# Kernel optimization log

Hardware: AMD Instinct MI355X
Metric: run time of the kernel (lower is better)

The kernel has to match this reference:

```python
import jax, jax.numpy as jnp
import numpy as np

G = 17          # joint groups == deform_groups == conv groups
BN_EPS = 1e-5   # torch BatchNorm2d default eps


def setup_inputs() -> dict:
    key = jax.random.key(0)
    ks = jax.random.split(key, 4)
    B, C, H, W = 4, 544, 96, 96
    Cg = C // G
    x = jax.random.normal(ks[0], (B, C, H, W), jnp.float32)
    # small std so sampled offsets stay a few pixels (realistic post-training scale)
    w_off = jax.random.normal(ks[1], (6 * G, Cg, 3, 3), jnp.float32) * 0.01
    b_off = jnp.zeros((6 * G,), jnp.float32)
    w_def = jax.random.normal(ks[2], (C, Cg, 3, 3), jnp.float32) * 0.05
    gamma = jnp.ones((C,), jnp.float32)
    beta = jnp.zeros((C,), jnp.float32)
    run_mean = jnp.zeros((C,), jnp.float32)
    run_var = jnp.ones((C,), jnp.float32)
    return dict(x=x, w_off=w_off, b_off=b_off, w_def=w_def, gamma=gamma,
                beta=beta, run_mean=run_mean, run_var=run_var)


def _forward(x, w_off, b_off, w_def, gamma, beta, run_mean, run_var):
    B, C, H, W = x.shape
    Cg = C // G
    residual = x
    # --- offset generation: grouped 3x3 conv -> per-pixel 2x3 affine per group ---
    t = jax.lax.conv_general_dilated(
        x, w_off, window_strides=(1, 1), padding=((1, 1), (1, 1)),
        dimension_numbers=('NCHW', 'OIHW', 'NCHW'), feature_group_count=G)
    t = t + b_off[None, :, None, None]
    aff = t.transpose(0, 2, 3, 1).reshape(B, H, W, G, 2, 3)   # [B,H,W,G,2,3]
    # regular 3x3 grid in homogeneous coords: rows = (dy, dx, 1), 9 taps row-major
    reg = jnp.array([[-1, -1, -1, 0, 0, 0, 1, 1, 1],
                     [-1, 0, 1, -1, 0, 1, -1, 0, 1],
                     [1, 1, 1, 1, 1, 1, 1, 1, 1]], jnp.float32)
    off = jnp.einsum('bhwgrt,tk->bhwgrk', aff, reg)           # [B,H,W,G,2,9]
    off = off.transpose(0, 3, 5, 1, 2, 4)                     # [B,G,9,H,W,2]
    offy = off[..., 0]                                        # [B,G,9,H,W]
    offx = off[..., 1]
    # --- deformable conv: bilinear-sampled gather at offset grid taps ---
    ky = jnp.array([-1, -1, -1, 0, 0, 0, 1, 1, 1], jnp.float32)
    kx = jnp.array([-1, 0, 1, -1, 0, 1, -1, 0, 1], jnp.float32)
    hh = jnp.arange(H, dtype=jnp.float32)
    ww = jnp.arange(W, dtype=jnp.float32)
    py = hh[None, None, None, :, None] + ky[None, None, :, None, None] + offy
    px = ww[None, None, None, None, :] + kx[None, None, :, None, None] + offx
    xf = x.reshape(B, G, Cg, H * W)
    y0 = jnp.floor(py)
    x0 = jnp.floor(px)
    sampled = jnp.zeros((B, G, Cg, 9, H, W), x.dtype)
    for dy in (0.0, 1.0):
        for dx in (0.0, 1.0):
            yc = y0 + dy
            xc = x0 + dx
            wgt = (1.0 - jnp.abs(py - yc)) * (1.0 - jnp.abs(px - xc))
            valid = ((yc >= 0) & (yc < H) & (xc >= 0) & (xc < W)).astype(x.dtype)
            yi = jnp.clip(yc, 0, H - 1).astype(jnp.int32)
            xi = jnp.clip(xc, 0, W - 1).astype(jnp.int32)
            idx = (yi * W + xi).reshape(B, G, 1, 9 * H * W)
            v = jnp.take_along_axis(xf, idx, axis=3).reshape(B, G, Cg, 9, H, W)
            sampled = sampled + v * (wgt * valid)[:, :, None]
    wg = w_def.reshape(G, C // G, Cg, 9)                      # [G, Cout/G, Cin/G, 9]
    out = jnp.einsum('bgikhw,goik->bgohw', sampled, wg).reshape(B, C, H, W)
    # --- eval-mode BatchNorm2d + residual ReLU ---
    inv = jax.lax.rsqrt(run_var + BN_EPS)
    out = (out - run_mean[None, :, None, None]) * (inv * gamma)[None, :, None, None] \
          + beta[None, :, None, None]
    return jax.nn.relu(out + residual)


def reference(x, w_off, b_off, w_def, gamma, beta, run_mean, run_var):
    return _forward(x, w_off, b_off, w_def, gamma, beta, run_mean, run_var)
```

## Files before the change

kernel.cpp:

```cpp
#include <hip/hip_runtime.h>
#include <math.h>

#define G  17
#define Cg 32
#define B  4
#define C  544
#define H  96
#define W  96
#define HW (H*W)
#define TILES 36
#define NBLK (B*G*TILES)
#define BN_EPS 1e-5f

typedef float    f32x4  __attribute__((ext_vector_type(4)));
typedef short    short8 __attribute__((ext_vector_type(8)));
typedef _Float16 h2     __attribute__((ext_vector_type(2)));
typedef _Float16 h8     __attribute__((ext_vector_type(8)));

#define WIN       22
#define HALO      3
#define WPOS      (WIN*WIN)
#define W_STRIDE  80
#define W_BYTES   (WPOS*W_STRIDE)
#define B_STRIDE  592
#define B_BYTES   (Cg*B_STRIDE)
#define WO_BYTES  (6*B_STRIDE)
#define SMEM_BYTES (W_BYTES + B_BYTES + WO_BYTES)

__device__ __forceinline__ int swizzle_blk(int blk) {
    return (blk & 7) * (NBLK / 8) + (blk >> 3);
}

__global__ __launch_bounds__(256) void transpose_kernel(
    const float* __restrict__ x, _Float16* __restrict__ xT)
{
    __shared__ float t[256*33];
    const int blk  = swizzle_blk(blockIdx.x);
    const int tile = blk % TILES;
    const int g    = (blk / TILES) % G;
    const int b    = blk / (TILES*G);

    const float* xg = x + ((size_t)b*C + g*Cg)*HW + tile*256;
    #pragma unroll
    for (int i = 0; i < Cg; ++i)
        t[threadIdx.x*33 + i] = xg[(size_t)i*HW + threadIdx.x];
    __syncthreads();

    h8* dst = (h8*)(xT + ((size_t)(b*G + g)*HW + (size_t)tile*256)*Cg);
    #pragma unroll
    for (int r = 0; r < 4; ++r) {
        const int idx = r*256 + threadIdx.x;
        const float* s = &t[(idx >> 2)*33 + (idx & 3)*8];
        h8 o;
        #pragma unroll
        for (int j = 0; j < 8; ++j) o[j] = (_Float16)s[j];
        dst[idx] = o;
    }
}

__global__ __launch_bounds__(256) void fused_deform_kernel(
    const float* __restrict__ x, const _Float16* __restrict__ xT,
    const float* __restrict__ w_off, const float* __restrict__ b_off,
    const float* __restrict__ w_def, const float* __restrict__ gamma,
    const float* __restrict__ beta, const float* __restrict__ rmean,
    const float* __restrict__ rvar, float* __restrict__ out)
{
    __shared__ __align__(16) char smem[SMEM_BYTES];
    char* Wsm  = smem;
    char* Bsm  = smem + W_BYTES;
    char* Wo   = smem + W_BYTES + B_BYTES;
    char* AffS = Wo;

    const int blk  = swizzle_blk(blockIdx.x);
    const int tile = blk % TILES;
    const int g    = (blk / TILES) % G;
    const int b    = blk / (TILES*G);
    const int ty   = tile / 6, tx = tile % 6;
    const int h0   = ty*16,    w0 = tx*16;
    const int tid  = threadIdx.x;
    const int lane = tid & 63;
    const int wv   = tid >> 6;
    const int r15  = lane & 15;
    const int koff = lane >> 4;
    const int kb   = koff*16;

    const _Float16* xgT_base = xT + (size_t)(b*G + g)*HW*Cg;

    for (int i = tid; i < WPOS*4; i += 256) {
        const int pos = i >> 2, ch = (i & 3)*8;
        const int wy = pos / WIN, wx = pos % WIN;
        const int y  = h0 + wy - HALO, xx = w0 + wx - HALO;
        short8 v = (short8){0,0,0,0,0,0,0,0};
        if (((unsigned)y < H) && ((unsigned)xx < W))
            v = *(const short8*)(xgT_base + ((size_t)y*W + xx)*Cg + ch);
        *(short8*)(Wsm + pos*W_STRIDE + ch*2) = v;
    }
    for (int l = tid; l < Cg*288; l += 256) {
        const int o = l / 288, K = l % 288;
        const int t = K >> 5, i = K & 31;
        const float wt = w_def[(size_t)(g*Cg + o)*(Cg*9) + i*9 + t];
        *(_Float16*)(Bsm + o*B_STRIDE + K*2) = (_Float16)wt;
    }
    for (int l = tid; l < 6*288; l += 256) {
        const int o = l / 288, K = l % 288;
        const int t = K >> 5, i = K & 31;
        const float wt = w_off[(size_t)(g*6 + o)*288 + i*9 + t];
        *(_Float16*)(Wo + o*B_STRIDE + K*2) = (_Float16)wt;
    }
    __syncthreads();

    f32x4 acc_off[4];
    #pragma unroll
    for (int m = 0; m < 4; ++m) acc_off[m] = (f32x4){0.f, 0.f, 0.f, 0.f};

    #pragma unroll
    for (int t = 0; t < 9; ++t) {
        const int dy = t/3 - 1, dx = t%3 - 1;
        h8 bo = (h8){0,0,0,0,0,0,0,0};
        if (r15 < 6) bo = *(const h8*)(Wo + r15*B_STRIDE + t*64 + kb);
        #pragma unroll
        for (int m = 0; m < 4; ++m) {
            const int wr = wv*4 + m + dy + HALO;
            const int wc = r15 + dx + HALO;
            const h8 a = *(const h8*)(Wsm + (wr*WIN + wc)*W_STRIDE + kb);
            acc_off[m] = __builtin_amdgcn_mfma_f32_16x16x32_f16(a, bo, acc_off[m], 0, 0, 0);
        }
    }
    __syncthreads();

    if (r15 < 6) {
        #pragma unroll
        for (int m = 0; m < 4; ++m)
            #pragma unroll
            for (int r = 0; r < 4; ++r) {
                const int lp = (wv*4 + m)*16 + koff*4 + r;
                *(_Float16*)(AffS + lp*12 + r15*2) = (_Float16)acc_off[m][r];
            }
    }
    __syncthreads();

    const float bo0 = b_off[g*6+0], bo1 = b_off[g*6+1], bo2 = b_off[g*6+2];
    const float bo3 = b_off[g*6+3], bo4 = b_off[g*6+4], bo5 = b_off[g*6+5];
    float a0p[4], a1v[4], a2w[4], a3v[4], a4p[4], a5w[4];
    #pragma unroll
    for (int m = 0; m < 4; ++m) {
        const int row = wv*4 + m;
        const int lp = row*16 + r15;
        const h2 p01 = *(const h2*)(AffS + lp*12);
        const h2 p23 = *(const h2*)(AffS + lp*12 + 4);
        const h2 p45 = *(const h2*)(AffS + lp*12 + 8);
        a0p[m] = (float)p01[0] + bo0 + 1.0f;
        a1v[m] = (float)p01[1] + bo1;
        a2w[m] = (float)p23[0] + bo2 + (float)(row + HALO);
        a3v[m] = (float)p23[1] + bo3;
        a4p[m] = (float)p45[0] + bo4 + 1.0f;
        a5w[m] = (float)p45[1] + bo5 + (float)(r15 + HALO);
    }

    f32x4 acc[4][2];
    #pragma unroll
    for (int m = 0; m < 4; ++m)
        #pragma unroll
        for (int n = 0; n < 2; ++n)
            acc[m][n] = (f32x4){0.f, 0.f, 0.f, 0.f};

    #pragma unroll 1
    for (int t = 0; t < 9; ++t) {
        const float kyf = (float)(t/3 - 1);
        const float kxf = (float)(t%3 - 1);

        h8 af[4];
        #pragma unroll
        for (int m = 0; m < 4; ++m) {
            const float pyw = fmaf(a0p[m], kyf, fmaf(a1v[m], kxf, a2w[m]));
            const float pxw = fmaf(a3v[m], kyf, fmaf(a4p[m], kxf, a5w[m]));
            const float y0f = floorf(pyw), x0f = floorf(pxw);
            const float fy = pyw - y0f,   fx = pxw - x0f;
            int iy = (int)y0f, ix = (int)x0f;
            iy = min(max(iy, 0), WIN-2);
            ix = min(max(ix, 0), WIN-2);
            const float gy = 1.0f - fy, gx = 1.0f - fx;
            const float w00 = gy*gx, w01 = gy*fx, w10 = fy*gx, w11 = fy*fx;
            const _Float16 h00 = (_Float16)w00, h01 = (_Float16)w01;
            const _Float16 h10 = (_Float16)w10, h11 = (_Float16)w11;
            const h2 W00 = (h2){h00, h00}, W01 = (h2){h01, h01};
            const h2 W10 = (h2){h10, h10}, W11 = (h2){h11, h11};

            const char* base = Wsm + (iy*WIN + ix)*W_STRIDE + kb;
            union { short8 s; h2 h[4]; h8 v; } u00, u01, u10, u11, r;
            u00.s = *(const short8*)(base);
            u01.s = *(const short8*)(base + W_STRIDE);
            u10.s = *(const short8*)(base + WIN*W_STRIDE);
            u11.s = *(const short8*)(base + WIN*W_STRIDE + W_STRIDE);

            #pragma unroll
            for (int j = 0; j < 4; ++j)
                r.h[j] = W00*u00.h[j] + W01*u01.h[j] + W10*u10.h[j] + W11*u11.h[j];
            af[m] = r.v;
        }

        #pragma unroll
        for (int n = 0; n < 2; ++n) {
            const h8 bf = *(const h8*)(Bsm + (n*16 + r15)*B_STRIDE + t*64 + kb);
            #pragma unroll
            for (int m = 0; m < 4; ++m)
                acc[m][n] = __builtin_amdgcn_mfma_f32_16x16x32_f16(af[m], bf, acc[m][n], 0, 0, 0);
        }
    }

    float scl[2], shf[2];
    #pragma unroll
    for (int n = 0; n < 2; ++n) {
        const int c = g*Cg + n*16 + r15;
        const float inv = rsqrtf(rvar[c] + BN_EPS);
        scl[n] = inv * gamma[c];
        shf[n] = beta[c] - rmean[c]*scl[n];
    }
    #pragma unroll
    for (int m = 0; m < 4; ++m) {
        const int row = wv*4 + m;
        const int pxg = (h0 + row)*W + w0 + koff*4;
        #pragma unroll
        for (int n = 0; n < 2; ++n) {
            const int c = g*Cg + n*16 + r15;
            const size_t base = ((size_t)b*C + c)*HW + pxg;
            const float4 res = *(const float4*)(x + base);
            float4 ov;
            ov.x = fmaxf(fmaf(acc[m][n][0], scl[n], shf[n]) + res.x, 0.0f);
            ov.y = fmaxf(fmaf(acc[m][n][1], scl[n], shf[n]) + res.y, 0.0f);
            ov.z = fmaxf(fmaf(acc[m][n][2], scl[n], shf[n]) + res.z, 0.0f);
            ov.w = fmaxf(fmaf(acc[m][n][3], scl[n], shf[n]) + res.w, 0.0f);
            *(float4*)(out + base) = ov;
        }
    }
}

__global__ __launch_bounds__(256) void offset_conv_kernel(
    const float* __restrict__ x, const float* __restrict__ w_off,
    const float* __restrict__ b_off, float* __restrict__ aff)
{
    __shared__ float wl[Cg*9*6];
    const int blk  = swizzle_blk(blockIdx.x);
    const int tile = blk % TILES;
    const int g    = (blk / TILES) % G;
    const int b    = blk / (TILES*G);

    for (int l = threadIdx.x; l < Cg*9*6; l += 256) {
        int c = l % 6; int t = (l/6) % 9; int i = l/54;
        wl[l] = w_off[(size_t)(g*6 + c)*(Cg*9) + i*9 + t];
    }
    __syncthreads();

    const int p = tile*256 + threadIdx.x;
    const int h = p / W, w = p % W;

    float acc[6];
    #pragma unroll
    for (int c = 0; c < 6; ++c) acc[c] = b_off[g*6 + c];

    const float* xg = x + ((size_t)b*C + g*Cg)*HW;
    for (int i = 0; i < Cg; ++i) {
        const float* xc = xg + (size_t)i*HW;
        #pragma unroll
        for (int t = 0; t < 9; ++t) {
            const int dy = t/3 - 1, dx = t%3 - 1;
            const int yy = h + dy, xx = w + dx;
            float v = (yy >= 0 && yy < H && xx >= 0 && xx < W) ? xc[yy*W + xx] : 0.0f;
            #pragma unroll
            for (int c = 0; c < 6; ++c)
                acc[c] = fmaf(v, wl[(i*9 + t)*6 + c], acc[c]);
        }
    }

    float* ap = aff + ((size_t)(b*G + g)*6)*HW + p;
    #pragma unroll
    for (int c = 0; c < 6; ++c) ap[(size_t)c*HW] = acc[c];
}

__global__ __launch_bounds__(256) void deform_conv_kernel(
    const float* __restrict__ x, const float* __restrict__ w_def,
    const float* __restrict__ aff, const float* __restrict__ gamma,
    const float* __restrict__ beta, const float* __restrict__ rmean,
    const float* __restrict__ rvar, float* __restrict__ out)
{
    __shared__ float wl[9*Cg*Cg];
    const int blk  = swizzle_blk(blockIdx.x);
    const int tile = blk % TILES;
    const int g    = (blk / TILES) % G;
    const int b    = blk / (TILES*G);

    for (int l = threadIdx.x; l < 9*Cg*Cg; l += 256) {
        int o = l & 31; int i = (l >> 5) & 31; int k = l >> 10;
        wl[l] = w_def[(size_t)(g*Cg + o)*(Cg*9) + i*9 + k];
    }
    __syncthreads();

    const int p = tile*256 + threadIdx.x;
    const int h = p / W, w = p % W;

    const float* ap = aff + ((size_t)(b*G + g)*6)*HW + p;
    const float a0 = ap[0*(size_t)HW], a1 = ap[1*(size_t)HW], a2 = ap[2*(size_t)HW];
    const float a3 = ap[3*(size_t)HW], a4 = ap[4*(size_t)HW], a5 = ap[5*(size_t)HW];

    float acc[Cg];
    #pragma unroll
    for (int o = 0; o < Cg; ++o) acc[o] = 0.0f;

    const float* xg = x + ((size_t)b*C + g*Cg)*HW;

    #pragma unroll
    for (int k = 0; k < 9; ++k) {
        const float kyf = (float)(k/3 - 1);
        const float kxf = (float)(k%3 - 1);
        const float offy = a0*kyf + a1*kxf + a2;
        const float offx = a3*kyf + a4*kxf + a5;
        const float py = (float)h + kyf + offy;
        const float px = (float)w + kxf + offx;
        const float y0f = floorf(py), x0f = floorf(px);
        const float fy = py - y0f,   fx = px - x0f;
        const int y0 = (int)y0f, x0 = (int)x0f;
        const int y1 = y0 + 1,   x1 = x0 + 1;
        const bool vy0 = (y0 >= 0) && (y0 < H);
        const bool vy1 = (y1 >= 0) && (y1 < H);
        const bool vx0 = (x0 >= 0) && (x0 < W);
        const bool vx1 = (x1 >= 0) && (x1 < W);
        const float w00 = (vy0 && vx0) ? (1.0f - fy)*(1.0f - fx) : 0.0f;
        const float w01 = (vy0 && vx1) ? (1.0f - fy)*fx          : 0.0f;
        const float w10 = (vy1 && vx0) ? fy*(1.0f - fx)          : 0.0f;
        const float w11 = (vy1 && vx1) ? fy*fx                   : 0.0f;
        const int y0c = min(max(y0, 0), H-1), y1c = min(max(y1, 0), H-1);
        const int x0c = min(max(x0, 0), W-1), x1c = min(max(x1, 0), W-1);
        const int p00 = y0c*W + x0c, p01 = y0c*W + x1c;
        const int p10 = y1c*W + x0c, p11 = y1c*W + x1c;

        const float* wk = &wl[k*Cg*Cg];
        for (int i = 0; i < Cg; ++i) {
            const float* xc = xg + (size_t)i*HW;
            const float v = w00*xc[p00] + w01*xc[p01] + w10*xc[p10] + w11*xc[p11];
            #pragma unroll
            for (int o = 0; o < Cg; ++o)
                acc[o] = fmaf(v, wk[i*Cg + o], acc[o]);
        }
    }

    float* op = out + ((size_t)b*C + g*Cg)*HW + p;
    #pragma unroll
    for (int o = 0; o < Cg; ++o) {
        const int c = g*Cg + o;
        const float inv = rsqrtf(rvar[c] + BN_EPS);
        float val = (acc[o] - rmean[c]) * (inv * gamma[c]) + beta[c];
        val += xg[(size_t)o*HW + p];
        op[(size_t)o*HW] = fmaxf(val, 0.0f);
    }
}

extern "C" void kernel_launch(void* const* d_in, const int* in_sizes, int n_in,
                              void* d_out, int out_size, void* d_ws, size_t ws_size,
                              hipStream_t stream) {
    const float* x     = (const float*)d_in[0];
    const float* w_off = (const float*)d_in[1];
    const float* b_off = (const float*)d_in[2];
    const float* w_def = (const float*)d_in[3];
    const float* gamma = (const float*)d_in[4];
    const float* beta  = (const float*)d_in[5];
    const float* rmean = (const float*)d_in[6];
    const float* rvar  = (const float*)d_in[7];
    float* out = (float*)d_out;

    const size_t XT_BYTES  = (size_t)B*G*HW*Cg*sizeof(_Float16);
    const size_t AFF_BYTES = (size_t)B*G*6*HW*sizeof(float);

    if (ws_size >= XT_BYTES) {
        _Float16* xT = (_Float16*)d_ws;
        transpose_kernel<<<NBLK, 256, 0, stream>>>(x, xT);
        fused_deform_kernel<<<NBLK, 256, 0, stream>>>(x, xT, w_off, b_off,
                                                      w_def, gamma, beta,
                                                      rmean, rvar, out);
    } else if (ws_size >= AFF_BYTES) {
        float* aff = (float*)d_ws;
        offset_conv_kernel<<<NBLK, 256, 0, stream>>>(x, w_off, b_off, aff);
        deform_conv_kernel<<<NBLK, 256, 0, stream>>>(x, w_def, aff, gamma, beta,
                                                     rmean, rvar, out);
    }
}
```

Before: 114.1 us.

## Fuse NCHW-to-fp16 window staging into deform kernel, drop transpose pass

Removes the separate transpose kernel that wrote an fp16 channel-last copy of x to workspace. The fused kernel now loads the halo window straight from NCHW fp32 x with float4 row reads, converts to fp16 and scatters into the channel-interleaved shared layout. The aim is to save one kernel launch and a full write plus reread of the transposed tensor. In exchange, shared-memory stores become scattered 2-byte writes that may bank-conflict, and halo pixels are reread from fp32 by neighbouring tiles. The fallback two-kernel path is deleted.

```diff
diff --git a/kernel.cpp b/kernel.cpp
--- a/kernel.cpp
+++ b/kernel.cpp
@@ -31,39 +31,12 @@
     return (blk & 7) * (NBLK / 8) + (blk >> 3);
 }
 
-__global__ __launch_bounds__(256) void transpose_kernel(
-    const float* __restrict__ x, _Float16* __restrict__ xT)
-{
-    __shared__ float t[256*33];
-    const int blk  = swizzle_blk(blockIdx.x);
-    const int tile = blk % TILES;
-    const int g    = (blk / TILES) % G;
-    const int b    = blk / (TILES*G);
-
-    const float* xg = x + ((size_t)b*C + g*Cg)*HW + tile*256;
-    #pragma unroll
-    for (int i = 0; i < Cg; ++i)
-        t[threadIdx.x*33 + i] = xg[(size_t)i*HW + threadIdx.x];
-    __syncthreads();
-
-    h8* dst = (h8*)(xT + ((size_t)(b*G + g)*HW + (size_t)tile*256)*Cg);
-    #pragma unroll
-    for (int r = 0; r < 4; ++r) {
-        const int idx = r*256 + threadIdx.x;
-        const float* s = &t[(idx >> 2)*33 + (idx & 3)*8];
-        h8 o;
-        #pragma unroll
-        for (int j = 0; j < 8; ++j) o[j] = (_Float16)s[j];
-        dst[idx] = o;
-    }
-}
-
 __global__ __launch_bounds__(256) void fused_deform_kernel(
-    const float* __restrict__ x, const _Float16* __restrict__ xT,
-    const float* __restrict__ w_off, const float* __restrict__ b_off,
-    const float* __restrict__ w_def, const float* __restrict__ gamma,
-    const float* __restrict__ beta, const float* __restrict__ rmean,
-    const float* __restrict__ rvar, float* __restrict__ out)
+    const float* __restrict__ x, const float* __restrict__ w_off,
+    const float* __restrict__ b_off, const float* __restrict__ w_def,
+    const float* __restrict__ gamma, const float* __restrict__ beta,
+    const float* __restrict__ rmean, const float* __restrict__ rvar,
+    float* __restrict__ out)
 {
     __shared__ __align__(16) char smem[SMEM_BYTES];
     char* Wsm  = smem;
@@ -84,16 +57,34 @@
     const int koff = lane >> 4;
     const int kb   = koff*16;
 
-    const _Float16* xgT_base = xT + (size_t)(b*G + g)*HW*Cg;
-
-    for (int i = tid; i < WPOS*4; i += 256) {
-        const int pos = i >> 2, ch = (i & 3)*8;
-        const int wy = pos / WIN, wx = pos % WIN;
-        const int y  = h0 + wy - HALO, xx = w0 + wx - HALO;
-        short8 v = (short8){0,0,0,0,0,0,0,0};
-        if (((unsigned)y < H) && ((unsigned)xx < W))
-            v = *(const short8*)(xgT_base + ((size_t)y*W + xx)*Cg + ch);
-        *(short8*)(Wsm + pos*W_STRIDE + ch*2) = v;
+    const float* xg = x + ((size_t)b*C + g*Cg)*HW;
+
+    for (int i = tid; i < 32*22*6; i += 256) {
+        const int ch  = i / 132;
+        const int rem = i - ch*132;
+        const int wy  = rem / 6;
+        const int seg = rem - wy*6;
+        const int y   = h0 + wy - HALO;
+        const int cb  = w0 - 4 + seg*4;
+        f32x4 v = (f32x4){0.f, 0.f, 0.f, 0.f};
+        if ((unsigned)y < H) {
+            if (cb >= 0 && cb + 3 < W) {
+                v = *(const f32x4*)(xg + (size_t)ch*HW + y*W + cb);
+            } else {
+                const float* row = xg + (size_t)ch*HW + y*W;
+                #pragma unroll
+                for (int j = 0; j < 4; ++j) {
+                    const int c = cb + j;
+                    if ((unsigned)c < W) v[j] = row[c];
+                }
+            }
+        }
+        #pragma unroll
+        for (int j = 0; j < 4; ++j) {
+            const int wx = seg*4 + j - 1;
+            if ((unsigned)wx < WIN)
+                *(_Float16*)(Wsm + (wy*WIN + wx)*W_STRIDE + ch*2) = (_Float16)v[j];
+        }
     }
     for (int l = tid; l < Cg*288; l += 256) {
         const int o = l / 288, K = l % 288;
@@ -235,125 +226,6 @@
     }
 }
 
-__global__ __launch_bounds__(256) void offset_conv_kernel(
-    const float* __restrict__ x, const float* __restrict__ w_off,
-    const float* __restrict__ b_off, float* __restrict__ aff)
-{
-    __shared__ float wl[Cg*9*6];
-    const int blk  = swizzle_blk(blockIdx.x);
-    const int tile = blk % TILES;
-    const int g    = (blk / TILES) % G;
-    const int b    = blk / (TILES*G);
-
-    for (int l = threadIdx.x; l < Cg*9*6; l += 256) {
-        int c = l % 6; int t = (l/6) % 9; int i = l/54;
-        wl[l] = w_off[(size_t)(g*6 + c)*(Cg*9) + i*9 + t];
-    }
-    __syncthreads();
-
-    const int p = tile*256 + threadIdx.x;
-    const int h = p / W, w = p % W;
-
-    float acc[6];
-    #pragma unroll
-    for (int c = 0; c < 6; ++c) acc[c] = b_off[g*6 + c];
-
-    const float* xg = x + ((size_t)b*C + g*Cg)*HW;
-    for (int i = 0; i < Cg; ++i) {
-        const float* xc = xg + (size_t)i*HW;
-        #pragma unroll
-        for (int t = 0; t < 9; ++t) {
-            const int dy = t/3 - 1, dx = t%3 - 1;
-            const int yy = h + dy, xx = w + dx;
-            float v = (yy >= 0 && yy < H && xx >= 0 && xx < W) ? xc[yy*W + xx] : 0.0f;
-            #pragma unroll
-            for (int c = 0; c < 6; ++c)
-                acc[c] = fmaf(v, wl[(i*9 + t)*6 + c], acc[c]);
-        }
-    }
-
-    float* ap = aff + ((size_t)(b*G + g)*6)*HW + p;
-    #pragma unroll
-    for (int c = 0; c < 6; ++c) ap[(size_t)c*HW] = acc[c];
-}
-
-__global__ __launch_bounds__(256) void deform_conv_kernel(
-    const float* __restrict__ x, const float* __restrict__ w_def,
-    const float* __restrict__ aff, const float* __restrict__ gamma,
-    const float* __restrict__ beta, const float* __restrict__ rmean,
-    const float* __restrict__ rvar, float* __restrict__ out)
-{
-    __shared__ float wl[9*Cg*Cg];
-    const int blk  = swizzle_blk(blockIdx.x);
-    const int tile = blk % TILES;
-    const int g    = (blk / TILES) % G;
-    const int b    = blk / (TILES*G);
-
-    for (int l = threadIdx.x; l < 9*Cg*Cg; l += 256) {
-        int o = l & 31; int i = (l >> 5) & 31; int k = l >> 10;
-        wl[l] = w_def[(size_t)(g*Cg + o)*(Cg*9) + i*9 + k];
-    }
-    __syncthreads();
-
-    const int p = tile*256 + threadIdx.x;
-    const int h = p / W, w = p % W;
-
-    const float* ap = aff + ((size_t)(b*G + g)*6)*HW + p;
-    const float a0 = ap[0*(size_t)HW], a1 = ap[1*(size_t)HW], a2 = ap[2*(size_t)HW];
-    const float a3 = ap[3*(size_t)HW], a4 = ap[4*(size_t)HW], a5 = ap[5*(size_t)HW];
-
-    float acc[Cg];
-    #pragma unroll
-    for (int o = 0; o < Cg; ++o) acc[o] = 0.0f;
-
-    const float* xg = x + ((size_t)b*C + g*Cg)*HW;
-
-    #pragma unroll
-    for (int k = 0; k < 9; ++k) {
-        const float kyf = (float)(k/3 - 1);
-        const float kxf = (float)(k%3 - 1);
-        const float offy = a0*kyf + a1*kxf + a2;
-        const float offx = a3*kyf + a4*kxf + a5;
-        const float py = (float)h + kyf + offy;
-        const float px = (float)w + kxf + offx;
-        const float y0f = floorf(py), x0f = floorf(px);
-        const float fy = py - y0f,   fx = px - x0f;
-        const int y0 = (int)y0f, x0 = (int)x0f;
-        const int y1 = y0 + 1,   x1 = x0 + 1;
-        const bool vy0 = (y0 >= 0) && (y0 < H);
-        const bool vy1 = (y1 >= 0) && (y1 < H);
-        const bool vx0 = (x0 >= 0) && (x0 < W);
-        const bool vx1 = (x1 >= 0) && (x1 < W);
-        const float w00 = (vy0 && vx0) ? (1.0f - fy)*(1.0f - fx) : 0.0f;
-        const float w01 = (vy0 && vx1) ? (1.0f - fy)*fx          : 0.0f;
-        const float w10 = (vy1 && vx0) ? fy*(1.0f - fx)          : 0.0f;
-        const float w11 = (vy1 && vx1) ? fy*fx                   : 0.0f;
-        const int y0c = min(max(y0, 0), H-1), y1c = min(max(y1, 0), H-1);
-        const int x0c = min(max(x0, 0), W-1), x1c = min(max(x1, 0), W-1);
-        const int p00 = y0c*W + x0c, p01 = y0c*W + x1c;
-        const int p10 = y1c*W + x0c, p11 = y1c*W + x1c;
-
-        const float* wk = &wl[k*Cg*Cg];
-        for (int i = 0; i < Cg; ++i) {
-            const float* xc = xg + (size_t)i*HW;
-            const float v = w00*xc[p00] + w01*xc[p01] + w10*xc[p10] + w11*xc[p11];
-            #pragma unroll
-            for (int o = 0; o < Cg; ++o)
-                acc[o] = fmaf(v, wk[i*Cg + o], acc[o]);
-        }
-    }
-
-    float* op = out + ((size_t)b*C + g*Cg)*HW + p;
-    #pragma unroll
-    for (int o = 0; o < Cg; ++o) {
-        const int c = g*Cg + o;
-        const float inv = rsqrtf(rvar[c] + BN_EPS);
-        float val = (acc[o] - rmean[c]) * (inv * gamma[c]) + beta[c];
-        val += xg[(size_t)o*HW + p];
-        op[(size_t)o*HW] = fmaxf(val, 0.0f);
-    }
-}
-
 extern "C" void kernel_launch(void* const* d_in, const int* in_sizes, int n_in,
                               void* d_out, int out_size, void* d_ws, size_t ws_size,
                               hipStream_t stream) {
@@ -367,19 +239,8 @@
     const float* rvar  = (const float*)d_in[7];
     float* out = (float*)d_out;
 
-    const size_t XT_BYTES  = (size_t)B*G*HW*Cg*sizeof(_Float16);
-    const size_t AFF_BYTES = (size_t)B*G*6*HW*sizeof(float);
-
-    if (ws_size >= XT_BYTES) {
-        _Float16* xT = (_Float16*)d_ws;
-        transpose_kernel<<<NBLK, 256, 0, stream>>>(x, xT);
-        fused_deform_kernel<<<NBLK, 256, 0, stream>>>(x, xT, w_off, b_off,
-                                                      w_def, gamma, beta,
-                                                      rmean, rvar, out);
-    } else if (ws_size >= AFF_BYTES) {
-        float* aff = (float*)d_ws;
-        offset_conv_kernel<<<NBLK, 256, 0, stream>>>(x, w_off, b_off, aff);
-        deform_conv_kernel<<<NBLK, 256, 0, stream>>>(x, w_def, aff, gamma, beta,
-                                                     rmean, rvar, out);
-    }
+    (void)d_ws; (void)ws_size;
+
+    fused_deform_kernel<<<NBLK, 256, 0, stream>>>(x, w_off, b_off, w_def,
+                                                  gamma, beta, rmean, rvar, out);
 }
```

Result: slower. 122.9 us (+7.7%).

## Precompute fp16 weight tables in a prep kernel and read B-fragments from global memory

Applied to the files above, without the earlier changes.

A new prep kernel converts w_def and w_off once per call into fp16 tables laid out to match the MFMA K order, with the offset weights zero-padded to 16 rows. The fused kernel then stops staging weights in LDS and loads its B fragments straight from global memory, which are likely L2-resident. This removes the per-block strided fp32 weight gather and conversion, and shrinks LDS so more blocks can be resident. In exchange it adds a kernel launch, puts global-load latency inside the MFMA loop, and requires more workspace, falling back to the older path if the workspace is too small.

```diff
diff --git a/kernel.cpp b/kernel.cpp
--- a/kernel.cpp
+++ b/kernel.cpp
@@ -22,13 +22,33 @@
 #define WPOS      (WIN*WIN)
 #define W_STRIDE  80
 #define W_BYTES   (WPOS*W_STRIDE)
-#define B_STRIDE  592
-#define B_BYTES   (Cg*B_STRIDE)
-#define WO_BYTES  (6*B_STRIDE)
-#define SMEM_BYTES (W_BYTES + B_BYTES + WO_BYTES)
+#define AFFS_BYTES 3072
+#define SMEM_BYTES (W_BYTES + AFFS_BYTES)
+
+#define WDEFT_ELEMS (C*288)
+#define WOT_ELEMS   (G*16*288)
+#define PREP_ELEMS  (WDEFT_ELEMS + WOT_ELEMS)
 
 __device__ __forceinline__ int swizzle_blk(int blk) {
     return (blk & 7) * (NBLK / 8) + (blk >> 3);
+}
+
+__global__ __launch_bounds__(256) void prep_tables_kernel(
+    const float* __restrict__ w_def, const float* __restrict__ w_off,
+    _Float16* __restrict__ wdefT, _Float16* __restrict__ woT)
+{
+    const int idx = blockIdx.x*256 + threadIdx.x;
+    if (idx < WDEFT_ELEMS) {
+        const int K = idx % 288, c = idx / 288;
+        const int t = K >> 5, i = K & 31;
+        wdefT[idx] = (_Float16)w_def[(size_t)c*288 + i*9 + t];
+    } else if (idx < PREP_ELEMS) {
+        const int j = idx - WDEFT_ELEMS;
+        const int K = j % 288, o = (j / 288) % 16, g = j / (288*16);
+        const int t = K >> 5, i = K & 31;
+        const float v = (o < 6) ? w_off[(size_t)(g*6 + o)*288 + i*9 + t] : 0.0f;
+        woT[j] = (_Float16)v;
+    }
 }
 
 __global__ __launch_bounds__(256) void transpose_kernel(
@@ -60,16 +80,14 @@
 
 __global__ __launch_bounds__(256) void fused_deform_kernel(
     const float* __restrict__ x, const _Float16* __restrict__ xT,
-    const float* __restrict__ w_off, const float* __restrict__ b_off,
-    const float* __restrict__ w_def, const float* __restrict__ gamma,
+    const _Float16* __restrict__ wdefT, const _Float16* __restrict__ woT,
+    const float* __restrict__ b_off, const float* __restrict__ gamma,
     const float* __restrict__ beta, const float* __restrict__ rmean,
     const float* __restrict__ rvar, float* __restrict__ out)
 {
     __shared__ __align__(16) char smem[SMEM_BYTES];
     char* Wsm  = smem;
-    char* Bsm  = smem + W_BYTES;
-    char* Wo   = smem + W_BYTES + B_BYTES;
-    char* AffS = Wo;
+    char* AffS = smem + W_BYTES;
 
     const int blk  = swizzle_blk(blockIdx.x);
     const int tile = blk % TILES;
@@ -95,20 +113,9 @@
             v = *(const short8*)(xgT_base + ((size_t)y*W + xx)*Cg + ch);
         *(short8*)(Wsm + pos*W_STRIDE + ch*2) = v;
     }
-    for (int l = tid; l < Cg*288; l += 256) {
-        const int o = l / 288, K = l % 288;
-        const int t = K >> 5, i = K & 31;
-        const float wt = w_def[(size_t)(g*Cg + o)*(Cg*9) + i*9 + t];
-        *(_Float16*)(Bsm + o*B_STRIDE + K*2) = (_Float16)wt;
-    }
-    for (int l = tid; l < 6*288; l += 256) {
-        const int o = l / 288, K = l % 288;
-        const int t = K >> 5, i = K & 31;
-        const float wt = w_off[(size_t)(g*6 + o)*288 + i*9 + t];
-        *(_Float16*)(Wo + o*B_STRIDE + K*2) = (_Float16)wt;
-    }
-    __syncthreads();
-
+    __syncthreads();
+
+    const _Float16* woT_g = woT + (size_t)g*16*288 + r15*288 + koff*8;
     f32x4 acc_off[4];
     #pragma unroll
     for (int m = 0; m < 4; ++m) acc_off[m] = (f32x4){0.f, 0.f, 0.f, 0.f};
@@ -116,8 +123,7 @@
     #pragma unroll
     for (int t = 0; t < 9; ++t) {
         const int dy = t/3 - 1, dx = t%3 - 1;
-        h8 bo = (h8){0,0,0,0,0,0,0,0};
-        if (r15 < 6) bo = *(const h8*)(Wo + r15*B_STRIDE + t*64 + kb);
+        const h8 bo = *(const h8*)(woT_g + t*32);
         #pragma unroll
         for (int m = 0; m < 4; ++m) {
             const int wr = wv*4 + m + dy + HALO;
@@ -156,6 +162,9 @@
         a4p[m] = (float)p45[0] + bo4 + 1.0f;
         a5w[m] = (float)p45[1] + bo5 + (float)(r15 + HALO);
     }
+
+    const _Float16* wd_g0 = wdefT + ((size_t)(g*Cg) + r15)*288 + koff*8;
+    const _Float16* wd_g1 = wd_g0 + (size_t)16*288;
 
     f32x4 acc[4][2];
     #pragma unroll
@@ -199,12 +208,12 @@
             af[m] = r.v;
         }
 
-        #pragma unroll
-        for (int n = 0; n < 2; ++n) {
-            const h8 bf = *(const h8*)(Bsm + (n*16 + r15)*B_STRIDE + t*64 + kb);
-            #pragma unroll
-            for (int m = 0; m < 4; ++m)
-                acc[m][n] = __builtin_amdgcn_mfma_f32_16x16x32_f16(af[m], bf, acc[m][n], 0, 0, 0);
+        const h8 bf0 = *(const h8*)(wd_g0 + t*32);
+        const h8 bf1 = *(const h8*)(wd_g1 + t*32);
+        #pragma unroll
+        for (int m = 0; m < 4; ++m) {
+            acc[m][0] = __builtin_amdgcn_mfma_f32_16x16x32_f16(af[m], bf0, acc[m][0], 0, 0, 0);
+            acc[m][1] = __builtin_amdgcn_mfma_f32_16x16x32_f16(af[m], bf1, acc[m][1], 0, 0, 0);
         }
     }
 
@@ -367,15 +376,20 @@
     const float* rvar  = (const float*)d_in[7];
     float* out = (float*)d_out;
 
+    const size_t TBL_BYTES = 524288;
     const size_t XT_BYTES  = (size_t)B*G*HW*Cg*sizeof(_Float16);
     const size_t AFF_BYTES = (size_t)B*G*6*HW*sizeof(float);
 
-    if (ws_size >= XT_BYTES) {
-        _Float16* xT = (_Float16*)d_ws;
+    if (ws_size >= TBL_BYTES + XT_BYTES) {
+        _Float16* wdefT = (_Float16*)d_ws;
+        _Float16* woT   = wdefT + WDEFT_ELEMS;
+        _Float16* xT    = (_Float16*)((char*)d_ws + TBL_BYTES);
+
+        prep_tables_kernel<<<(PREP_ELEMS + 255)/256, 256, 0, stream>>>(
+            w_def, w_off, wdefT, woT);
         transpose_kernel<<<NBLK, 256, 0, stream>>>(x, xT);
-        fused_deform_kernel<<<NBLK, 256, 0, stream>>>(x, xT, w_off, b_off,
-                                                      w_def, gamma, beta,
-                                                      rmean, rvar, out);
+        fused_deform_kernel<<<NBLK, 256, 0, stream>>>(x, xT, wdefT, woT, b_off,
+                                                      gamma, beta, rmean, rvar, out);
     } else if (ws_size >= AFF_BYTES) {
         float* aff = (float*)d_ws;
         offset_conv_kernel<<<NBLK, 256, 0, stream>>>(x, w_off, b_off, aff);
```

After: 99.19 us. 13.1% less time.
